# Optimization experiments

Hardware: AMD Instinct MI355X
Metric: run time of the kernel (lower is better)

The kernel has to match this reference:

```python
import jax, jax.numpy as jnp
import numpy as np

H = 768          # hidden_size
HH = H // 2      # 384


def setup_inputs() -> dict:
    key = jax.random.key(0)
    ks = jax.random.split(key, 16)
    B, W, E, R = 32, 512, 128, 1024
    inp = {
        "hidden_states": jax.random.normal(ks[0], (B, W, H), dtype=jnp.float32),
        "relation_head": jax.random.randint(ks[1], (B, R), 0, E),
        "relation_tail": jax.random.randint(ks[2], (B, R), 0, E),
        "relation_label": jax.random.randint(ks[3], (B, R), 0, 2),
        "entities_start": jax.random.randint(ks[4], (B, E), 0, W),
        "entities_end": jax.random.randint(ks[5], (B, E), 0, W),
        "entities_label": jax.random.randint(ks[6], (B, E), 0, 3),
        # parameters (torch Linear convention: weight [out, in])
        "entity_emb": jax.random.normal(ks[7], (3, H), dtype=jnp.float32) * 0.02,
        "Wh1": jax.random.normal(ks[8], (H, 2 * H), dtype=jnp.float32) * 0.02,
        "bh1": jnp.zeros((H,), jnp.float32),
        "Wh2": jax.random.normal(ks[9], (HH, H), dtype=jnp.float32) * 0.02,
        "bh2": jnp.zeros((HH,), jnp.float32),
        "Wt1": jax.random.normal(ks[10], (H, 2 * H), dtype=jnp.float32) * 0.02,
        "bt1": jnp.zeros((H,), jnp.float32),
        "Wt2": jax.random.normal(ks[11], (HH, H), dtype=jnp.float32) * 0.02,
        "bt2": jnp.zeros((HH,), jnp.float32),
        "W_bil": jax.random.normal(ks[12], (2, HH, HH), dtype=jnp.float32) * 0.02,
        "W_lin": jax.random.normal(ks[13], (2, 2 * HH), dtype=jnp.float32) * 0.02,
        "b_lin": jnp.zeros((2,), jnp.float32),
    }
    return inp


def _ffnn(x, W1, b1, W2, b2):
    # two-layer MLP with ReLU (dropout is identity in eval mode)
    h = jax.nn.relu(jnp.einsum('brd,hd->brh', x, W1) + b1)
    return jax.nn.relu(jnp.einsum('brh,oh->bro', h, W2) + b2)


def reference(hidden_states, relation_head, relation_tail, relation_label,
              entities_start, entities_end, entities_label,
              entity_emb, Wh1, bh1, Wh2, bh2, Wt1, bt1, Wt2, bt2,
              W_bil, W_lin, b_lin):
    # gather per-relation entity info: [B, R]
    head_index = jnp.take_along_axis(entities_start, relation_head, axis=1)
    head_label = jnp.take_along_axis(entities_label, relation_head, axis=1)
    tail_index = jnp.take_along_axis(entities_start, relation_tail, axis=1)
    tail_label = jnp.take_along_axis(entities_label, relation_tail, axis=1)

    # gather token reprs: [B, R, H]
    head_tok = jnp.take_along_axis(hidden_states, head_index[:, :, None], axis=1)
    tail_tok = jnp.take_along_axis(hidden_states, tail_index[:, :, None], axis=1)

    head_repr = jnp.concatenate([head_tok, entity_emb[head_label]], axis=-1)  # [B,R,2H]
    tail_repr = jnp.concatenate([tail_tok, entity_emb[tail_label]], axis=-1)

    heads = _ffnn(head_repr, Wh1, bh1, Wh2, bh2)  # [B,R,HH]
    tails = _ffnn(tail_repr, Wt1, bt1, Wt2, bt2)

    # biaffine: bilinear + linear on concat
    bil = jnp.einsum('bri,oij,brj->bro', heads, W_bil, tails)
    lin = jnp.einsum('brc,oc->bro', jnp.concatenate([heads, tails], axis=-1), W_lin) + b_lin
    logits = bil + lin  # [B, R, 2]

    # per-doc mean CE summed over docs
    logp = jax.nn.log_softmax(logits, axis=-1)
    nll = -jnp.take_along_axis(logp, relation_label[:, :, None], axis=-1)[..., 0]  # [B,R]
    loss = jnp.sum(jnp.mean(nll, axis=1))
    return loss
```

## Files before the change

kernel.cpp:

```cpp
#include <hip/hip_runtime.h>
#include <math.h>

typedef unsigned short u16;
typedef __bf16 bf16x8 __attribute__((ext_vector_type(8)));
typedef float f32x4 __attribute__((ext_vector_type(4)));

#define B_ 32
#define W_ 512
#define H_ 768
#define HH_ 384
#define E_ 128
#define R_ 1024
#define BE_ (B_*E_)
#define K1_ (2*H_)

__device__ __forceinline__ u16 f2bf(float f) {
  unsigned u = __float_as_uint(f);
  u = (u + 0x7fffu + ((u >> 16) & 1u)) >> 16;
  return (u16)u;
}
__device__ __forceinline__ float bf2f(u16 u) {
  return __uint_as_float(((unsigned)u) << 16);
}

__device__ __forceinline__ void gload_lds16(const void* g, void* l) {
  __builtin_amdgcn_global_load_lds(
      (__attribute__((address_space(1))) void*)(g),
      (__attribute__((address_space(3))) void*)(l), 16, 0, 0);
}

__device__ __forceinline__ void xcd_swizzle(int& bx, int& by) {
  const int nwg = gridDim.x * gridDim.y;
  int orig = blockIdx.y * gridDim.x + blockIdx.x;
  int q = nwg >> 3, r = nwg & 7;
  int xcd = orig & 7, idx = orig >> 3;
  int wgid = (xcd < r ? xcd * (q + 1) : r * (q + 1) + (xcd - r) * q) + idx;
  bx = wgid % gridDim.x;
  by = wgid / gridDim.x;
}

#define NBLK_W 2017
#define NBLK_P 1152
#define NBLK_X 4096

__global__ __launch_bounds__(256) void prep_all(
    const float* __restrict__ Wh1, const float* __restrict__ Wt1,
    const float* __restrict__ Wh2, const float* __restrict__ Wt2,
    const float* __restrict__ Wbil,
    const float* __restrict__ bh1, const float* __restrict__ bt1,
    const float* __restrict__ bh2, const float* __restrict__ bt2,
    const float* __restrict__ emb,
    const float* __restrict__ hs, const int* __restrict__ ent_start,
    u16* __restrict__ W1c, u16* __restrict__ W2c, u16* __restrict__ Wb,
    float* __restrict__ b2cat, float* __restrict__ P, u16* __restrict__ X)
{
  const int blk = blockIdx.x;
  const int tid = threadIdx.x;

  if (blk < NBLK_W) {
    const int i = blk * 256 + tid;
    const int SW1 = 294912;
    const int SW2 = SW1 + 147456;
    const int SWB = SW2 + 73728;
    const int SB2 = SWB + 192;
    if (i < SW1) {
      int row = i / 192, c = i % 192;
      const float4* src = (const float4*)((row < 768)
          ? (Wh1 + (size_t)row * K1_) : (Wt1 + (size_t)(row - 768) * K1_));
      float4 v = src[c];
      ushort4 o; o.x = f2bf(v.x); o.y = f2bf(v.y); o.z = f2bf(v.z); o.w = f2bf(v.w);
      ((ushort4*)W1c)[i] = o;
    } else if (i < SW2) {
      int j = i - SW1;
      float4 v = (j < 73728) ? ((const float4*)Wh2)[j]
                             : ((const float4*)Wt2)[j - 73728];
      ushort4 o; o.x = f2bf(v.x); o.y = f2bf(v.y); o.z = f2bf(v.z); o.w = f2bf(v.w);
      ((ushort4*)W2c)[j] = o;
    } else if (i < SWB) {
      int j = i - SW2;
      float4 v = ((const float4*)Wbil)[j];
      ushort4 o; o.x = f2bf(v.x); o.y = f2bf(v.y); o.z = f2bf(v.z); o.w = f2bf(v.w);
      ((ushort4*)Wb)[j] = o;
    } else if (i < SB2) {
      int j = i - SWB;
      ((float4*)b2cat)[j] = (j < 96) ? ((const float4*)bh2)[j]
                                     : ((const float4*)bt2)[j - 96];
    }
  } else if (blk < NBLK_W + NBLK_P) {
    const int w = (blk - NBLK_W) * 4 + (tid >> 6);
    const int lane = tid & 63;
    const int l = w / K1_;
    const int n = w - l * K1_;
    const float* wrow = (n < 768) ? (Wh1 + (size_t)n * K1_ + 768)
                                  : (Wt1 + (size_t)(n - 768) * K1_ + 768);
    const float  bb   = (n < 768) ? bh1[n] : bt1[n - 768];
    const float* ev = emb + (size_t)l * H_;
    float s = 0.f;
#pragma unroll
    for (int t = 0; t < 12; ++t) {
      int d = lane + 64 * t;
      s += ev[d] * wrow[d];
    }
#pragma unroll
    for (int off = 32; off; off >>= 1) s += __shfl_down(s, off);
    if (lane == 0) P[(size_t)l * K1_ + n] = s + bb;
  } else {
    const int be = blk - (NBLK_W + NBLK_P);
    if (tid < 192) {
      int b = be >> 7;
      int start = ent_start[be];
      const float4* s0 = (const float4*)(hs + ((size_t)b * W_ + start) * H_);
      float4 v = s0[tid];
      ushort4 o; o.x = f2bf(v.x); o.y = f2bf(v.y); o.z = f2bf(v.z); o.w = f2bf(v.w);
      ((ushort4*)(X + (size_t)be * H_))[tid] = o;
    }
  }
}

#define BM 128
#define BN 128
#define BKK 64

__global__ __launch_bounds__(256, 2) void gemm_bf16(
    const u16* __restrict__ A, int lda,
    const u16* __restrict__ Wt,
    const float* __restrict__ bias,
    u16* __restrict__ C, int ldc,
    int M, int N, int K, int do_relu, int half_n, int aoff,
    const float* __restrict__ rowBias,
    const int* __restrict__ rowLabel, int ldP)
{
  __shared__ char smem[2 * BM * (BKK * 2)];
  char* As = smem;
  char* Bs = smem + BM * BKK * 2;

  int bx, by;
  xcd_swizzle(bx, by);
  const int bn = bx * BN;
  const int bm = by * BM;

  const int tid  = threadIdx.x;
  const int wid  = tid >> 6;
  const int lane = tid & 63;
  const int wm = ((wid >> 1) & 1) * 64;
  const int wn = (wid & 1) * 64;

  const int a0 = (half_n && bn >= half_n) ? aoff : 0;

  const int srow = lane >> 3;
  const int sk8  = (lane & 7) ^ srow;
  const u16* gA = A  + (size_t)(bm + 32*wid + srow) * lda + a0 + 8*sk8;
  const u16* gB = Wt + (size_t)(bn + 32*wid + srow) * K  + 8*sk8;

  const int frow = lane & 15;
  const int fk8  = lane >> 4;

  f32x4 acc[4][4] = {};

  for (int k0 = 0; k0 < K; k0 += BKK) {
#pragma unroll
    for (int i = 0; i < 4; ++i) {
      gload_lds16(gA + (size_t)i * 8 * lda, As + (4*wid + i) * 1024);
      gload_lds16(gB + (size_t)i * 8 * K,   Bs + (4*wid + i) * 1024);
    }
    gA += BKK; gB += BKK;
    asm volatile("s_waitcnt vmcnt(0)" ::: "memory");
    __syncthreads();

#pragma unroll
    for (int kh = 0; kh < 2; ++kh) {
      bf16x8 a[4], b[4];
#pragma unroll
      for (int m = 0; m < 4; ++m) {
        const int row  = wm + m*16 + frow;
        const int slot = (kh*4 + fk8) ^ (row & 7);
        a[m] = *(const bf16x8*)(As + row*128 + slot*16);
      }
#pragma unroll
      for (int n = 0; n < 4; ++n) {
        const int row  = wn + n*16 + frow;
        const int slot = (kh*4 + fk8) ^ (row & 7);
        b[n] = *(const bf16x8*)(Bs + row*128 + slot*16);
      }
#pragma unroll
      for (int m = 0; m < 4; ++m)
#pragma unroll
        for (int n = 0; n < 4; ++n)
          acc[m][n] = __builtin_amdgcn_mfma_f32_16x16x32_bf16(
              a[m], b[n], acc[m][n], 0, 0, 0);
    }
    __syncthreads();
  }

  int lbl[4][4];
  if (rowLabel) {
#pragma unroll
    for (int m = 0; m < 4; ++m)
#pragma unroll
      for (int r = 0; r < 4; ++r)
        lbl[m][r] = rowLabel[bm + wm + m*16 + fk8*4 + r];
  }

#pragma unroll
  for (int n = 0; n < 4; ++n) {
    const int col = bn + wn + n*16 + frow;
    const float bv = bias ? bias[col] : 0.f;
    float p0 = 0.f, p1 = 0.f, p2 = 0.f;
    if (rowLabel) {
      p0 = rowBias[col];
      p1 = rowBias[ldP + col];
      p2 = rowBias[2*ldP + col];
    }
#pragma unroll
    for (int m = 0; m < 4; ++m) {
#pragma unroll
      for (int r = 0; r < 4; ++r) {
        const int row = bm + wm + m*16 + fk8*4 + r;
        float v = acc[m][n][r] + bv;
        if (rowLabel) {
          int l = lbl[m][r];
          v += (l == 0) ? p0 : ((l == 1) ? p1 : p2);
        }
        if (do_relu) v = fmaxf(v, 0.f);
        C[(size_t)row * ldc + col] = f2bf(v);
      }
    }
  }
}

__global__ __launch_bounds__(256, 2) void gemm_S(
    const u16* __restrict__ Hcat, const u16* __restrict__ U,
    const float* __restrict__ linHT, const float* __restrict__ b_lin,
    float* __restrict__ S)
{
  __shared__ char smem[2 * 128 * 128];
  char* As = smem;
  char* Bs = smem + 128 * 128;

  int bx, by;
  xcd_swizzle(bx, by);
  const int z  = by;
  const int bn = bx * 128;

  const int tid  = threadIdx.x;
  const int wid  = tid >> 6;
  const int lane = tid & 63;
  const int wm = ((wid >> 1) & 1) * 64;
  const int wn = (wid & 1) * 64;

  const int srow = lane >> 3;
  const int sk8  = (lane & 7) ^ srow;
  const u16* gA = Hcat + (size_t)z * 128 * 768 + (size_t)(32*wid + srow) * 768 + 8*sk8;
  const u16* gB = U    + (size_t)z * 128 * 768 + (size_t)(bn + 32*wid + srow) * 384 + 8*sk8;

  const int frow = lane & 15;
  const int fk8  = lane >> 4;

  f32x4 acc[4][4] = {};

  for (int k0 = 0; k0 < 384; k0 += BKK) {
#pragma unroll
    for (int i = 0; i < 4; ++i) {
      gload_lds16(gA + (size_t)i * 8 * 768, As + (4*wid + i) * 1024);
      gload_lds16(gB + (size_t)i * 8 * 384, Bs + (4*wid + i) * 1024);
    }
    gA += BKK; gB += BKK;
    asm volatile("s_waitcnt vmcnt(0)" ::: "memory");
    __syncthreads();

#pragma unroll
    for (int kh = 0; kh < 2; ++kh) {
      bf16x8 a[4], b[4];
#pragma unroll
      for (int m = 0; m < 4; ++m) {
        const int row  = wm + m*16 + frow;
        const int slot = (kh*4 + fk8) ^ (row & 7);
        a[m] = *(const bf16x8*)(As + row*128 + slot*16);
      }
#pragma unroll
      for (int n = 0; n < 4; ++n) {
        const int row  = wn + n*16 + frow;
        const int slot = (kh*4 + fk8) ^ (row & 7);
        b[n] = *(const bf16x8*)(Bs + row*128 + slot*16);
      }
#pragma unroll
      for (int m = 0; m < 4; ++m)
#pragma unroll
        for (int n = 0; n < 4; ++n)
          acc[m][n] = __builtin_amdgcn_mfma_f32_16x16x32_bf16(
              a[m], b[n], acc[m][n], 0, 0, 0);
    }
    __syncthreads();
  }

  const int o = (bn + wn + frow) & 1;
  const float blv = b_lin[o];
  float linHrow[4][4];
#pragma unroll
  for (int m = 0; m < 4; ++m)
#pragma unroll
    for (int r = 0; r < 4; ++r)
      linHrow[m][r] = linHT[(size_t)(z*128 + wm + m*16 + fk8*4 + r) * 4 + o];

#pragma unroll
  for (int n = 0; n < 4; ++n) {
    const int n_out = bn + wn + n*16 + frow;
    const int e2 = n_out >> 1;
    const float lt = linHT[(size_t)(z*128 + e2) * 4 + 2 + o];
#pragma unroll
    for (int m = 0; m < 4; ++m) {
#pragma unroll
      for (int r = 0; r < 4; ++r) {
        const int row = wm + m*16 + fk8*4 + r;
        S[((size_t)(z*128 + row)) * 256 + n_out] =
            acc[m][n][r] + linHrow[m][r] + lt + blv;
      }
    }
  }
}

__global__ __launch_bounds__(128) void lin_parts_kernel(
    const u16* __restrict__ Hcat, const float* __restrict__ W_lin,
    float* __restrict__ linHT, float* __restrict__ out)
{
  if (blockIdx.x == 0 && threadIdx.x == 0) out[0] = 0.f;
  int be   = blockIdx.x;
  int wid  = threadIdx.x >> 6;
  int lane = threadIdx.x & 63;
  const u16* src = Hcat + (size_t)be * (2*HH_) + wid * HH_;
  const float* wl0 = W_lin + (wid ? HH_ : 0);
  const float* wl1 = W_lin + 2*HH_ + (wid ? HH_ : 0);
  float s0 = 0.f, s1 = 0.f;
#pragma unroll
  for (int t = 0; t < HH_/64; ++t) {
    int i = lane + t*64;
    float v = bf2f(src[i]);
    s0 += v * wl0[i];
    s1 += v * wl1[i];
  }
#pragma unroll
  for (int off = 32; off; off >>= 1) {
    s0 += __shfl_down(s0, off);
    s1 += __shfl_down(s1, off);
  }
  if (lane == 0) {
    linHT[be*4 + wid*2 + 0] = s0;
    linHT[be*4 + wid*2 + 1] = s1;
  }
}

__global__ __launch_bounds__(256) void ce_kernel(
    const int* __restrict__ rel_head, const int* __restrict__ rel_tail,
    const int* __restrict__ rel_label, const float* __restrict__ S,
    float* __restrict__ out)
{
  const int i = blockIdx.x * 256 + threadIdx.x;
  const int b  = i >> 10;
  const int rh = rel_head[i];
  const int rt = rel_tail[i];
  const int lab = rel_label[i];
  const float2 lv = *(const float2*)(S + ((size_t)(b*E_ + rh)) * 256 + rt*2);
  const float l0 = lv.x, l1 = lv.y;
  const float m = fmaxf(l0, l1);
  const float lse = m + logf(expf(l0 - m) + expf(l1 - m));
  float nll = lse - (lab == 0 ? l0 : l1);

#pragma unroll
  for (int off = 32; off; off >>= 1) nll += __shfl_down(nll, off);
  __shared__ float red[4];
  if ((threadIdx.x & 63) == 0) red[threadIdx.x >> 6] = nll;
  __syncthreads();
  if (threadIdx.x == 0)
    atomicAdd(out, (red[0] + red[1] + red[2] + red[3]) * (1.0f / R_));
}

extern "C" void kernel_launch(void* const* d_in, const int* in_sizes, int n_in,
                              void* d_out, int out_size, void* d_ws, size_t ws_size,
                              hipStream_t stream)
{
  const float* hs        = (const float*)d_in[0];
  const int*   rel_head  = (const int*)  d_in[1];
  const int*   rel_tail  = (const int*)  d_in[2];
  const int*   rel_label = (const int*)  d_in[3];
  const int*   ent_start = (const int*)  d_in[4];
  const int*   ent_label = (const int*)  d_in[6];
  const float* emb   = (const float*)d_in[7];
  const float* Wh1   = (const float*)d_in[8];
  const float* bh1   = (const float*)d_in[9];
  const float* Wh2   = (const float*)d_in[10];
  const float* bh2   = (const float*)d_in[11];
  const float* Wt1   = (const float*)d_in[12];
  const float* bt1   = (const float*)d_in[13];
  const float* Wt2   = (const float*)d_in[14];
  const float* bt2   = (const float*)d_in[15];
  const float* W_bil = (const float*)d_in[16];
  const float* W_lin = (const float*)d_in[17];
  const float* b_lin = (const float*)d_in[18];
  float* out = (float*)d_out;

  u16* X    = (u16*)d_ws;
  u16* H1   = X    + (size_t)BE_ * H_;
  u16* Hcat = H1   + (size_t)BE_ * K1_;
  u16* U    = Hcat + (size_t)BE_ * H_;
  u16* W1c  = U    + (size_t)BE_ * H_;
  u16* W2c  = W1c  + (size_t)K1_ * H_;
  u16* Wb   = W2c  + (size_t)H_ * H_;
  float* b2cat = (float*)(Wb + (size_t)H_ * HH_);
  float* P     = b2cat + H_;
  float* linHT = P + 3*K1_;
  float* S     = linHT + 4*BE_;

  prep_all<<<dim3(NBLK_W + NBLK_P + NBLK_X), dim3(256), 0, stream>>>(
      Wh1, Wt1, Wh2, Wt2, W_bil, bh1, bt1, bh2, bt2, emb,
      hs, ent_start, W1c, W2c, Wb, b2cat, P, X);

  gemm_bf16<<<dim3(K1_/BN, BE_/BM), dim3(256), 0, stream>>>(
      X, H_, W1c, (const float*)nullptr, H1, K1_, BE_, K1_, H_, 1, 0, 0,
      P, ent_label, K1_);

  gemm_bf16<<<dim3(H_/BN, BE_/BM), dim3(256), 0, stream>>>(
      H1, K1_, W2c, b2cat, Hcat, H_, BE_, H_, H_, 1, HH_, H_,
      (const float*)nullptr, (const int*)nullptr, 0);

  lin_parts_kernel<<<dim3(BE_), dim3(128), 0, stream>>>(Hcat, W_lin, linHT, out);

  gemm_bf16<<<dim3(H_/BN, BE_/BM), dim3(256), 0, stream>>>(
      Hcat + HH_, H_, Wb, (const float*)nullptr, U, H_, BE_, H_, HH_, 0, 0, 0,
      (const float*)nullptr, (const int*)nullptr, 0);

  gemm_S<<<dim3(2, B_), dim3(256), 0, stream>>>(Hcat, U, linHT, b_lin, S);

  ce_kernel<<<dim3(B_*R_/256), dim3(256), 0, stream>>>(
      rel_head, rel_tail, rel_label, S, out);
}
```

Measured before the change: 75.73 us.

## Double-buffer GEMM LDS loads, retile gemm_S smaller, vectorize lin_parts

```diff
diff --git a/kernel.cpp b/kernel.cpp
--- a/kernel.cpp
+++ b/kernel.cpp
@@ -130,9 +130,7 @@
     const float* __restrict__ rowBias,
     const int* __restrict__ rowLabel, int ldP)
 {
-  __shared__ char smem[2 * BM * (BKK * 2)];
-  char* As = smem;
-  char* Bs = smem + BM * BKK * 2;
+  __shared__ char smem[2 * 32768];
 
   int bx, by;
   xcd_swizzle(bx, by);
@@ -157,16 +155,27 @@
 
   f32x4 acc[4][4] = {};
 
-  for (int k0 = 0; k0 < K; k0 += BKK) {
+  auto stage = [&](int buf, int k0) {
+    char* As = smem + buf * 32768;
+    char* Bs = As + 16384;
 #pragma unroll
     for (int i = 0; i < 4; ++i) {
-      gload_lds16(gA + (size_t)i * 8 * lda, As + (4*wid + i) * 1024);
-      gload_lds16(gB + (size_t)i * 8 * K,   Bs + (4*wid + i) * 1024);
-    }
-    gA += BKK; gB += BKK;
-    asm volatile("s_waitcnt vmcnt(0)" ::: "memory");
-    __syncthreads();
-
+      gload_lds16(gA + k0 + (size_t)i * 8 * lda, As + (4*wid + i) * 1024);
+      gload_lds16(gB + k0 + (size_t)i * 8 * K,   Bs + (4*wid + i) * 1024);
+    }
+  };
+
+  const int nt = K / BKK;
+  stage(0, 0);
+  asm volatile("s_waitcnt vmcnt(0)" ::: "memory");
+  __syncthreads();
+
+  for (int t = 0; t < nt; ++t) {
+    const int cur = t & 1;
+    if (t + 1 < nt) stage(cur ^ 1, (t + 1) * BKK);
+
+    char* As = smem + cur * 32768;
+    char* Bs = As + 16384;
 #pragma unroll
     for (int kh = 0; kh < 2; ++kh) {
       bf16x8 a[4], b[4];
@@ -189,7 +198,11 @@
           acc[m][n] = __builtin_amdgcn_mfma_f32_16x16x32_bf16(
               a[m], b[n], acc[m][n], 0, 0, 0);
     }
-    __syncthreads();
+
+    if (t + 1 < nt) {
+      asm volatile("s_waitcnt vmcnt(0)" ::: "memory");
+      __syncthreads();
+    }
   }
 
   int lbl[4][4];
@@ -233,119 +246,141 @@
     const float* __restrict__ linHT, const float* __restrict__ b_lin,
     float* __restrict__ S)
 {
-  __shared__ char smem[2 * 128 * 128];
-  char* As = smem;
-  char* Bs = smem + 128 * 128;
+  __shared__ char smem[2 * 16384];
 
   int bx, by;
   xcd_swizzle(bx, by);
-  const int z  = by;
-  const int bn = bx * 128;
+  const int z  = by >> 1;
+  const int bm = (by & 1) * 64;
+  const int bn = bx * 64;
 
   const int tid  = threadIdx.x;
   const int wid  = tid >> 6;
   const int lane = tid & 63;
-  const int wm = ((wid >> 1) & 1) * 64;
-  const int wn = (wid & 1) * 64;
+  const int wm = ((wid >> 1) & 1) * 32;
+  const int wn = (wid & 1) * 32;
 
   const int srow = lane >> 3;
   const int sk8  = (lane & 7) ^ srow;
-  const u16* gA = Hcat + (size_t)z * 128 * 768 + (size_t)(32*wid + srow) * 768 + 8*sk8;
-  const u16* gB = U    + (size_t)z * 128 * 768 + (size_t)(bn + 32*wid + srow) * 384 + 8*sk8;
+  const u16* gA = Hcat + (size_t)z * 98304 + (size_t)(bm + 16*wid + srow) * 768 + 8*sk8;
+  const u16* gB = U    + (size_t)z * 98304 + (size_t)(bn + 16*wid + srow) * 384 + 8*sk8;
 
   const int frow = lane & 15;
   const int fk8  = lane >> 4;
 
-  f32x4 acc[4][4] = {};
-
-  for (int k0 = 0; k0 < 384; k0 += BKK) {
-#pragma unroll
-    for (int i = 0; i < 4; ++i) {
-      gload_lds16(gA + (size_t)i * 8 * 768, As + (4*wid + i) * 1024);
-      gload_lds16(gB + (size_t)i * 8 * 384, Bs + (4*wid + i) * 1024);
-    }
-    gA += BKK; gB += BKK;
-    asm volatile("s_waitcnt vmcnt(0)" ::: "memory");
-    __syncthreads();
-
+  f32x4 acc[2][2] = {};
+
+  auto stage = [&](int buf, int k0) {
+    char* As = smem + buf * 16384;
+    char* Bs = As + 8192;
+#pragma unroll
+    for (int i = 0; i < 2; ++i) {
+      gload_lds16(gA + k0 + (size_t)i * 8 * 768, As + (2*wid + i) * 1024);
+      gload_lds16(gB + k0 + (size_t)i * 8 * 384, Bs + (2*wid + i) * 1024);
+    }
+  };
+
+  const int nt = 384 / BKK;
+  stage(0, 0);
+  asm volatile("s_waitcnt vmcnt(0)" ::: "memory");
+  __syncthreads();
+
+  for (int t = 0; t < nt; ++t) {
+    const int cur = t & 1;
+    if (t + 1 < nt) stage(cur ^ 1, (t + 1) * BKK);
+
+    char* As = smem + cur * 16384;
+    char* Bs = As + 8192;
 #pragma unroll
     for (int kh = 0; kh < 2; ++kh) {
-      bf16x8 a[4], b[4];
-#pragma unroll
-      for (int m = 0; m < 4; ++m) {
+      bf16x8 a[2], b[2];
+#pragma unroll
+      for (int m = 0; m < 2; ++m) {
         const int row  = wm + m*16 + frow;
         const int slot = (kh*4 + fk8) ^ (row & 7);
         a[m] = *(const bf16x8*)(As + row*128 + slot*16);
       }
 #pragma unroll
-      for (int n = 0; n < 4; ++n) {
+      for (int n = 0; n < 2; ++n) {
         const int row  = wn + n*16 + frow;
         const int slot = (kh*4 + fk8) ^ (row & 7);
         b[n] = *(const bf16x8*)(Bs + row*128 + slot*16);
       }
 #pragma unroll
-      for (int m = 0; m < 4; ++m)
-#pragma unroll
-        for (int n = 0; n < 4; ++n)
+      for (int m = 0; m < 2; ++m)
+#pragma unroll
+        for (int n = 0; n < 2; ++n)
           acc[m][n] = __builtin_amdgcn_mfma_f32_16x16x32_bf16(
               a[m], b[n], acc[m][n], 0, 0, 0);
     }
-    __syncthreads();
-  }
-
-  const int o = (bn + wn + frow) & 1;
+
+    if (t + 1 < nt) {
+      asm volatile("s_waitcnt vmcnt(0)" ::: "memory");
+      __syncthreads();
+    }
+  }
+
+  const int o = frow & 1;
   const float blv = b_lin[o];
-  float linHrow[4][4];
-#pragma unroll
-  for (int m = 0; m < 4; ++m)
+  float linH[2][4];
+#pragma unroll
+  for (int m = 0; m < 2; ++m)
 #pragma unroll
     for (int r = 0; r < 4; ++r)
-      linHrow[m][r] = linHT[(size_t)(z*128 + wm + m*16 + fk8*4 + r) * 4 + o];
-
-#pragma unroll
-  for (int n = 0; n < 4; ++n) {
+      linH[m][r] = linHT[(size_t)(z*128 + bm + wm + m*16 + fk8*4 + r) * 4 + o];
+
+#pragma unroll
+  for (int n = 0; n < 2; ++n) {
     const int n_out = bn + wn + n*16 + frow;
     const int e2 = n_out >> 1;
     const float lt = linHT[(size_t)(z*128 + e2) * 4 + 2 + o];
 #pragma unroll
-    for (int m = 0; m < 4; ++m) {
+    for (int m = 0; m < 2; ++m) {
 #pragma unroll
       for (int r = 0; r < 4; ++r) {
-        const int row = wm + m*16 + fk8*4 + r;
+        const int row = bm + wm + m*16 + fk8*4 + r;
         S[((size_t)(z*128 + row)) * 256 + n_out] =
-            acc[m][n][r] + linHrow[m][r] + lt + blv;
-      }
-    }
-  }
-}
-
-__global__ __launch_bounds__(128) void lin_parts_kernel(
+            acc[m][n][r] + linH[m][r] + lt + blv;
+      }
+    }
+  }
+}
+
+__global__ __launch_bounds__(256) void lin_parts_kernel(
     const u16* __restrict__ Hcat, const float* __restrict__ W_lin,
     float* __restrict__ linHT, float* __restrict__ out)
 {
   if (blockIdx.x == 0 && threadIdx.x == 0) out[0] = 0.f;
-  int be   = blockIdx.x;
-  int wid  = threadIdx.x >> 6;
-  int lane = threadIdx.x & 63;
-  const u16* src = Hcat + (size_t)be * (2*HH_) + wid * HH_;
-  const float* wl0 = W_lin + (wid ? HH_ : 0);
-  const float* wl1 = W_lin + 2*HH_ + (wid ? HH_ : 0);
-  float s0 = 0.f, s1 = 0.f;
-#pragma unroll
-  for (int t = 0; t < HH_/64; ++t) {
-    int i = lane + t*64;
-    float v = bf2f(src[i]);
-    s0 += v * wl0[i];
-    s1 += v * wl1[i];
-  }
-#pragma unroll
-  for (int off = 32; off; off >>= 1) {
-    s0 += __shfl_down(s0, off);
-    s1 += __shfl_down(s1, off);
-  }
-  if (lane == 0) {
-    linHT[be*4 + wid*2 + 0] = s0;
-    linHT[be*4 + wid*2 + 1] = s1;
+  const int wave = blockIdx.x * 4 + (threadIdx.x >> 6);
+  const int lane = threadIdx.x & 63;
+  const int nwave = gridDim.x * 4;
+
+  for (int be = wave; be < BE_; be += nwave) {
+    const ushort4* src = (const ushort4*)(Hcat + (size_t)be * 768);
+    float s0 = 0.f, s1 = 0.f, s2 = 0.f, s3 = 0.f;
+#pragma unroll
+    for (int rd = 0; rd < 3; ++rd) {
+      const int idx4 = rd * 64 + lane;
+      const int c = idx4 * 4;
+      ushort4 v4 = src[idx4];
+      float4 w0 = *(const float4*)(W_lin + c);
+      float4 w1 = *(const float4*)(W_lin + 768 + c);
+      float d0 = bf2f(v4.x)*w0.x + bf2f(v4.y)*w0.y + bf2f(v4.z)*w0.z + bf2f(v4.w)*w0.w;
+      float d1 = bf2f(v4.x)*w1.x + bf2f(v4.y)*w1.y + bf2f(v4.z)*w1.z + bf2f(v4.w)*w1.w;
+      if (c < 384) { s0 += d0; s1 += d1; }
+      else         { s2 += d0; s3 += d1; }
+    }
+#pragma unroll
+    for (int off = 32; off; off >>= 1) {
+      s0 += __shfl_down(s0, off);
+      s1 += __shfl_down(s1, off);
+      s2 += __shfl_down(s2, off);
+      s3 += __shfl_down(s3, off);
+    }
+    if (lane == 0) {
+      float4 v = {s0, s1, s2, s3};
+      *(float4*)(linHT + (size_t)be * 4) = v;
+    }
   }
 }
 
@@ -422,13 +457,13 @@
       H1, K1_, W2c, b2cat, Hcat, H_, BE_, H_, H_, 1, HH_, H_,
       (const float*)nullptr, (const int*)nullptr, 0);
 
-  lin_parts_kernel<<<dim3(BE_), dim3(128), 0, stream>>>(Hcat, W_lin, linHT, out);
+  lin_parts_kernel<<<dim3(128), dim3(256), 0, stream>>>(Hcat, W_lin, linHT, out);
 
   gemm_bf16<<<dim3(H_/BN, BE_/BM), dim3(256), 0, stream>>>(
       Hcat + HH_, H_, Wb, (const float*)nullptr, U, H_, BE_, H_, HH_, 0, 0, 0,
       (const float*)nullptr, (const int*)nullptr, 0);
 
-  gemm_S<<<dim3(2, B_), dim3(256), 0, stream>>>(Hcat, U, linHT, b_lin, S);
+  gemm_S<<<dim3(4, 2*B_), dim3(256), 0, stream>>>(Hcat, U, linHT, b_lin, S);
 
   ce_kernel<<<dim3(B_*R_/256), dim3(256), 0, stream>>>(
       rel_head, rel_tail, rel_label, S, out);
```

After: 68.35 us. 9.7% less time.
